# Performance work log

Hardware: AMD Instinct MI355X
Metric: run time of the kernel (lower is better)

Reference implementation:

```python
import jax, jax.numpy as jnp
import numpy as np

B, T, H = 2048, 200, 64
H1, H2 = 80, 40  # dnn_hidden_units


def setup_inputs() -> dict:
    key = jax.random.key(0)
    ks = jax.random.split(key, 9)
    query = jax.random.normal(ks[0], (B, H), dtype=jnp.float32)
    keys = jax.random.normal(ks[1], (B, T, H), dtype=jnp.float32)
    # lengths in [1, T] so every row has at least one valid key
    keys_length = jax.random.randint(ks[2], (B,), 1, T + 1, dtype=jnp.int32)
    s = 0.05  # weight scale (init_std in the repo is 1e-4; scaled up for numerics)
    W1 = jax.random.normal(ks[3], (4 * H, H1), dtype=jnp.float32) * s
    b1 = jnp.zeros((H1,), dtype=jnp.float32)
    W2 = jax.random.normal(ks[4], (H1, H2), dtype=jnp.float32) * s
    b2 = jnp.zeros((H2,), dtype=jnp.float32)
    Wfc = jax.random.normal(ks[5], (H2, 1), dtype=jnp.float32) * s
    bfc = jnp.zeros((1,), dtype=jnp.float32)
    return {"query": query, "keys": keys, "keys_length": keys_length,
            "W1": W1, "b1": b1, "W2": W2, "b2": b2, "Wfc": Wfc, "bfc": bfc}


def reference(query, keys, keys_length, W1, b1, W2, b2, Wfc, bfc):
    b, t, h = keys.shape
    qe = jnp.broadcast_to(query[:, None, :], keys.shape)          # [B,T,H]
    din = jnp.concatenate([qe, keys, qe - keys, qe * keys], -1)   # [B,T,4H]
    x = jax.nn.relu(jnp.einsum('btd,df->btf', din, W1) + b1)      # [B,T,H1]
    x = jax.nn.relu(jnp.einsum('btf,fg->btg', x, W2) + b2)        # [B,T,H2]
    scores = (jnp.einsum('btg,go->bto', x, Wfc) + bfc)[..., 0]    # [B,T]
    scores = scores / jnp.sqrt(jnp.float32(h))
    mask = jnp.arange(t)[None, :] < keys_length[:, None]          # [B,T]
    scores = jnp.where(mask, scores, -jnp.inf)
    attn = jax.nn.softmax(scores, axis=1)                         # [B,T]
    return jnp.einsum('bt,bth->bh', attn, keys)                   # [B,H]
```

## Files before the change

### kernel.cpp

```cpp
#include <hip/hip_runtime.h>
#include <math.h>

#define BB 2048
#define T  200
#define H  64
#define H1 80
#define H2 40

#define MT   13
#define TPAD 208
#define SA_STRIDE 72
#define SB1_STRIDE 72
#define SW_STRIDE 104
#define SB2_STRIDE 104

typedef __attribute__((ext_vector_type(8))) short short8;
typedef __attribute__((ext_vector_type(4))) float floatx4;

#define WS_WKT 0
#define WS_WPT (WS_WKT + H1 * H)
#define WS_WQ  (WS_WPT + H1 * H)
#define WS_W2T (WS_WQ + H * H1)

__device__ __forceinline__ unsigned short f2b(float x) {
    union { float f; unsigned u; } v; v.f = x;
    unsigned r = v.u + 0x7FFF + ((v.u >> 16) & 1);
    return (unsigned short)(r >> 16);
}
__device__ __forceinline__ float b2f(unsigned short u) {
    union { unsigned u; float f; } v; v.u = ((unsigned)u) << 16;
    return v.f;
}

__global__ void prep_kernel(const float* __restrict__ W1,
                            const float* __restrict__ W2,
                            float* __restrict__ ws) {
    int i = blockIdx.x * 256 + threadIdx.x;
    if (i < H1 * H) {
        int f = i / H, h = i % H;
        ws[WS_WKT + i] = W1[(64 + h) * H1 + f] - W1[(128 + h) * H1 + f];
        ws[WS_WPT + i] = W1[(192 + h) * H1 + f];
        ws[WS_WQ + h * H1 + f] = W1[h * H1 + f] + W1[(128 + h) * H1 + f];
    }
    if (i < 48 * SB2_STRIDE) {
        int n = i / SB2_STRIDE, k = i % SB2_STRIDE;
        float v = (n < H2 && k < H1) ? W2[k * H2 + n] : 0.f;
        ((unsigned short*)(ws + WS_W2T))[i] = f2b(v);
    }
}

__global__ __launch_bounds__(512, 4)
void din_attn_kernel(const float* __restrict__ query,
                     const float* __restrict__ keys,
                     const int*   __restrict__ keys_length,
                     const float* __restrict__ b1,
                     const float* __restrict__ b2,
                     const float* __restrict__ Wfc,
                     const float* __restrict__ bfc,
                     const float* __restrict__ ws,
                     float* __restrict__ out)
{
    __shared__ unsigned short sA[TPAD * SA_STRIDE];
    __shared__ unsigned short sHw[8][16 * SW_STRIDE];
    __shared__ unsigned short sB1[H1 * SB1_STRIDE];
    __shared__ float sQh[H1];
    __shared__ float sS[TPAD];
    __shared__ float sOut[8][H];
    __shared__ float sRed[16];

    const int b   = blockIdx.x;
    const int tid = threadIdx.x;
    const int wv  = tid >> 6, ln = tid & 63;
    const int lrow = ln & 15;
    const int lk8  = (ln >> 4) * 8;

    const float* kb = keys + (size_t)b * T * H;
    const float* qg = query + (size_t)b * H;

    const unsigned short* w2t = (const unsigned short*)(ws + WS_W2T);
    short8 b2frag[3][3];
    #pragma unroll
    for (int nt = 0; nt < 3; ++nt)
        #pragma unroll
        for (int ks = 0; ks < 3; ++ks)
            b2frag[nt][ks] = *reinterpret_cast<const short8*>(
                &w2t[(nt * 16 + lrow) * SB2_STRIDE + ks * 32 + lk8]);
    float wfcv[3], b2v[3];
    #pragma unroll
    for (int nt = 0; nt < 3; ++nt) {
        int g = nt * 16 + lrow;
        wfcv[nt] = (g < H2) ? Wfc[g] : 0.f;
        b2v[nt]  = (g < H2) ? b2[g]  : 0.f;
    }
    float bfc0 = bfc[0];
    int len = keys_length[b];

    for (int idx = tid; idx < T * H / 4; idx += 512) {
        float4 v = reinterpret_cast<const float4*>(kb)[idx];
        int t = idx >> 4, h = (idx & 15) << 2;
        uint2 p;
        p.x = (unsigned)f2b(v.x) | ((unsigned)f2b(v.y) << 16);
        p.y = (unsigned)f2b(v.z) | ((unsigned)f2b(v.w) << 16);
        *reinterpret_cast<uint2*>(&sA[t * SA_STRIDE + h]) = p;
    }
    for (int idx = tid; idx < 8 * SA_STRIDE / 2; idx += 512)
        reinterpret_cast<unsigned*>(&sA[200 * SA_STRIDE])[idx] = 0;
    for (int idx = tid; idx < H1 * H / 2; idx += 512) {
        int f = idx >> 5, hp = (idx & 31) << 1;
        float q0 = qg[hp], q1 = qg[hp + 1];
        float v0 = ws[WS_WKT + f * H + hp]     + q0 * ws[WS_WPT + f * H + hp];
        float v1 = ws[WS_WKT + f * H + hp + 1] + q1 * ws[WS_WPT + f * H + hp + 1];
        unsigned p = (unsigned)f2b(v0) | ((unsigned)f2b(v1) << 16);
        *reinterpret_cast<unsigned*>(&sB1[f * SB1_STRIDE + hp]) = p;
    }
    if (tid < H1) {
        float acc = b1[tid];
        #pragma unroll 8
        for (int h = 0; h < H; ++h) acc += qg[h] * ws[WS_WQ + h * H1 + tid];
        sQh[tid] = acc;
    }
    {
        uint2 z; z.x = 0; z.y = 0;
        *reinterpret_cast<uint2*>(&sHw[wv][lrow * SW_STRIDE + 80 + (ln >> 4) * 4]) = z;
    }
    __syncthreads();

    unsigned short* hw = &sHw[wv][0];
    #pragma unroll
    for (int mi = 0; mi < 2; ++mi) {
        int mt = wv + mi * 8;
        if (mt >= MT) break;
        short8 af[2];
        #pragma unroll
        for (int ks = 0; ks < 2; ++ks)
            af[ks] = *reinterpret_cast<const short8*>(
                &sA[(mt * 16 + lrow) * SA_STRIDE + ks * 32 + lk8]);
        #pragma unroll
        for (int nt = 0; nt < 5; ++nt) {
            short8 bf0 = *reinterpret_cast<const short8*>(
                &sB1[(nt * 16 + lrow) * SB1_STRIDE + lk8]);
            short8 bf1 = *reinterpret_cast<const short8*>(
                &sB1[(nt * 16 + lrow) * SB1_STRIDE + 32 + lk8]);
            floatx4 acc = {0.f, 0.f, 0.f, 0.f};
            acc = __builtin_amdgcn_mfma_f32_16x16x32_bf16(af[0], bf0, acc, 0, 0, 0);
            acc = __builtin_amdgcn_mfma_f32_16x16x32_bf16(af[1], bf1, acc, 0, 0, 0);
            float qh = sQh[nt * 16 + lrow];
            int rb = (ln >> 4) * 4;
            #pragma unroll
            for (int r = 0; r < 4; ++r)
                hw[(rb + r) * SW_STRIDE + nt * 16 + lrow] = f2b(fmaxf(acc[r] + qh, 0.f));
        }
        short8 a2[3];
        #pragma unroll
        for (int ks = 0; ks < 3; ++ks)
            a2[ks] = *reinterpret_cast<const short8*>(
                &hw[lrow * SW_STRIDE + ks * 32 + lk8]);
        floatx4 vsum = {0.f, 0.f, 0.f, 0.f};
        #pragma unroll
        for (int nt = 0; nt < 3; ++nt) {
            floatx4 acc = {0.f, 0.f, 0.f, 0.f};
            #pragma unroll
            for (int ks = 0; ks < 3; ++ks)
                acc = __builtin_amdgcn_mfma_f32_16x16x32_bf16(a2[ks], b2frag[nt][ks], acc, 0, 0, 0);
            #pragma unroll
            for (int r = 0; r < 4; ++r)
                vsum[r] += fmaxf(acc[r] + b2v[nt], 0.f) * wfcv[nt];
        }
        #pragma unroll
        for (int r = 0; r < 4; ++r) {
            vsum[r] += __shfl_xor(vsum[r], 1);
            vsum[r] += __shfl_xor(vsum[r], 2);
            vsum[r] += __shfl_xor(vsum[r], 4);
            vsum[r] += __shfl_xor(vsum[r], 8);
        }
        if (lrow == 0) {
            int tb = mt * 16 + (ln >> 4) * 4;
            #pragma unroll
            for (int r = 0; r < 4; ++r)
                sS[tb + r] = (vsum[r] + bfc0) * 0.125f;
        }
    }
    __syncthreads();

    float s = -INFINITY;
    if (tid < TPAD) s = (tid < len) ? sS[tid] : -INFINITY;
    float m = s;
    #pragma unroll
    for (int off = 32; off > 0; off >>= 1) m = fmaxf(m, __shfl_xor(m, off));
    if (ln == 0) sRed[wv] = m;
    __syncthreads();
    float mx = sRed[0];
    #pragma unroll
    for (int i = 1; i < 8; ++i) mx = fmaxf(mx, sRed[i]);
    float e = (tid < TPAD) ? __expf(s - mx) : 0.f;
    float sum = e;
    #pragma unroll
    for (int off = 32; off > 0; off >>= 1) sum += __shfl_xor(sum, off);
    if (ln == 0) sRed[8 + wv] = sum;
    __syncthreads();
    float denom = sRed[8];
    #pragma unroll
    for (int i = 1; i < 8; ++i) denom += sRed[8 + i];
    float inv = 1.f / denom;
    if (tid < TPAD) sS[tid] = e * inv;
    __syncthreads();

    float acc = 0.f;
    for (int t = wv * 26; t < wv * 26 + 26; ++t)
        acc += sS[t] * b2f(sA[t * SA_STRIDE + ln]);
    sOut[wv][ln] = acc;
    __syncthreads();
    if (tid < H) {
        float o = 0.f;
        #pragma unroll
        for (int g = 0; g < 8; ++g) o += sOut[g][tid];
        out[(size_t)b * H + tid] = o;
    }
}

extern "C" void kernel_launch(void* const* d_in, const int* in_sizes, int n_in,
                              void* d_out, int out_size, void* d_ws, size_t ws_size,
                              hipStream_t stream) {
    const float* query       = (const float*)d_in[0];
    const float* keys        = (const float*)d_in[1];
    const int*   keys_length = (const int*)  d_in[2];
    const float* W1          = (const float*)d_in[3];
    const float* b1          = (const float*)d_in[4];
    const float* W2          = (const float*)d_in[5];
    const float* b2          = (const float*)d_in[6];
    const float* Wfc         = (const float*)d_in[7];
    const float* bfc         = (const float*)d_in[8];
    float* out = (float*)d_out;
    float* ws  = (float*)d_ws;

    prep_kernel<<<20, 256, 0, stream>>>(W1, W2, ws);
    din_attn_kernel<<<BB, 512, 0, stream>>>(query, keys, keys_length,
                                            b1, b2, Wfc, bfc, ws, out);
}
```

Measured before the change: 60.36 us.

## Shrink LDS with XOR swizzle and buffer reuse to raise occupancy

```diff
diff --git a/kernel.cpp b/kernel.cpp
--- a/kernel.cpp
+++ b/kernel.cpp
@@ -9,10 +9,8 @@
 
 #define MT   13
 #define TPAD 208
-#define SA_STRIDE 72
-#define SB1_STRIDE 72
-#define SW_STRIDE 104
 #define SB2_STRIDE 104
+#define SCR_STRIDE 104
 
 typedef __attribute__((ext_vector_type(8))) short short8;
 typedef __attribute__((ext_vector_type(4))) float floatx4;
@@ -49,7 +47,7 @@
     }
 }
 
-__global__ __launch_bounds__(512, 4)
+__global__ __launch_bounds__(512, 6)
 void din_attn_kernel(const float* __restrict__ query,
                      const float* __restrict__ keys,
                      const int*   __restrict__ keys_length,
@@ -60,12 +58,10 @@
                      const float* __restrict__ ws,
                      float* __restrict__ out)
 {
-    __shared__ unsigned short sA[TPAD * SA_STRIDE];
-    __shared__ unsigned short sHw[8][16 * SW_STRIDE];
-    __shared__ unsigned short sB1[H1 * SB1_STRIDE];
+    __shared__ unsigned short sA[TPAD * 64];
+    __shared__ unsigned short sB1[H1 * 64];
     __shared__ float sQh[H1];
     __shared__ float sS[TPAD];
-    __shared__ float sOut[8][H];
     __shared__ float sRed[16];
 
     const int b   = blockIdx.x;
@@ -73,18 +69,12 @@
     const int wv  = tid >> 6, ln = tid & 63;
     const int lrow = ln & 15;
     const int lk8  = (ln >> 4) * 8;
+    const int sw   = (lrow & 7) << 3;
 
     const float* kb = keys + (size_t)b * T * H;
     const float* qg = query + (size_t)b * H;
-
     const unsigned short* w2t = (const unsigned short*)(ws + WS_W2T);
-    short8 b2frag[3][3];
-    #pragma unroll
-    for (int nt = 0; nt < 3; ++nt)
-        #pragma unroll
-        for (int ks = 0; ks < 3; ++ks)
-            b2frag[nt][ks] = *reinterpret_cast<const short8*>(
-                &w2t[(nt * 16 + lrow) * SB2_STRIDE + ks * 32 + lk8]);
+
     float wfcv[3], b2v[3];
     #pragma unroll
     for (int nt = 0; nt < 3; ++nt) {
@@ -95,23 +85,44 @@
     float bfc0 = bfc[0];
     int len = keys_length[b];
 
-    for (int idx = tid; idx < T * H / 4; idx += 512) {
-        float4 v = reinterpret_cast<const float4*>(kb)[idx];
+    const float4* kb4 = reinterpret_cast<const float4*>(kb);
+    float4 kv[6];
+    #pragma unroll
+    for (int k = 0; k < 6; ++k) kv[k] = kb4[tid + (k << 9)];
+    const bool tail = tid < (T * H / 4 - 3072);
+    float4 kvt;
+    if (tail) kvt = kb4[tid + 3072];
+
+    #pragma unroll
+    for (int k = 0; k < 6; ++k) {
+        int idx = tid + (k << 9);
         int t = idx >> 4, h = (idx & 15) << 2;
         uint2 p;
-        p.x = (unsigned)f2b(v.x) | ((unsigned)f2b(v.y) << 16);
-        p.y = (unsigned)f2b(v.z) | ((unsigned)f2b(v.w) << 16);
-        *reinterpret_cast<uint2*>(&sA[t * SA_STRIDE + h]) = p;
-    }
-    for (int idx = tid; idx < 8 * SA_STRIDE / 2; idx += 512)
-        reinterpret_cast<unsigned*>(&sA[200 * SA_STRIDE])[idx] = 0;
-    for (int idx = tid; idx < H1 * H / 2; idx += 512) {
+        p.x = (unsigned)f2b(kv[k].x) | ((unsigned)f2b(kv[k].y) << 16);
+        p.y = (unsigned)f2b(kv[k].z) | ((unsigned)f2b(kv[k].w) << 16);
+        *reinterpret_cast<uint2*>(&sA[t * 64 + (h ^ ((t & 7) << 3))]) = p;
+    }
+    if (tail) {
+        int idx = tid + 3072;
+        int t = idx >> 4, h = (idx & 15) << 2;
+        uint2 p;
+        p.x = (unsigned)f2b(kvt.x) | ((unsigned)f2b(kvt.y) << 16);
+        p.y = (unsigned)f2b(kvt.z) | ((unsigned)f2b(kvt.w) << 16);
+        *reinterpret_cast<uint2*>(&sA[t * 64 + (h ^ ((t & 7) << 3))]) = p;
+    }
+    if (tid < 64) {
+        uint4 z; z.x = z.y = z.z = z.w = 0;
+        reinterpret_cast<uint4*>(&sA[200 * 64])[tid] = z;
+    }
+    #pragma unroll
+    for (int k = 0; k < 5; ++k) {
+        int idx = tid + (k << 9);
         int f = idx >> 5, hp = (idx & 31) << 1;
         float q0 = qg[hp], q1 = qg[hp + 1];
         float v0 = ws[WS_WKT + f * H + hp]     + q0 * ws[WS_WPT + f * H + hp];
         float v1 = ws[WS_WKT + f * H + hp + 1] + q1 * ws[WS_WPT + f * H + hp + 1];
         unsigned p = (unsigned)f2b(v0) | ((unsigned)f2b(v1) << 16);
-        *reinterpret_cast<unsigned*>(&sB1[f * SB1_STRIDE + hp]) = p;
+        *reinterpret_cast<unsigned*>(&sB1[f * 64 + (hp ^ ((f & 7) << 3))]) = p;
     }
     if (tid < H1) {
         float acc = b1[tid];
@@ -119,49 +130,64 @@
         for (int h = 0; h < H; ++h) acc += qg[h] * ws[WS_WQ + h * H1 + tid];
         sQh[tid] = acc;
     }
+    __syncthreads();
+
+    short8 af[2][2];
+    bool has[2];
+    #pragma unroll
+    for (int mi = 0; mi < 2; ++mi) {
+        int mt = wv + mi * 8;
+        has[mi] = (mt < MT);
+        if (has[mi]) {
+            #pragma unroll
+            for (int ks = 0; ks < 2; ++ks) {
+                int row = mt * 16 + lrow;
+                af[mi][ks] = *reinterpret_cast<const short8*>(
+                    &sA[row * 64 + ((ks * 32 + lk8) ^ sw)]);
+            }
+        }
+    }
+    __syncthreads();
+
+    unsigned short* scr = &sA[wv * 16 * SCR_STRIDE];
     {
         uint2 z; z.x = 0; z.y = 0;
-        *reinterpret_cast<uint2*>(&sHw[wv][lrow * SW_STRIDE + 80 + (ln >> 4) * 4]) = z;
-    }
-    __syncthreads();
-
-    unsigned short* hw = &sHw[wv][0];
+        *reinterpret_cast<uint2*>(&scr[(ln >> 2) * SCR_STRIDE + 80 + (ln & 3) * 4]) = z;
+    }
+
     #pragma unroll
     for (int mi = 0; mi < 2; ++mi) {
+        if (!has[mi]) break;
         int mt = wv + mi * 8;
-        if (mt >= MT) break;
-        short8 af[2];
-        #pragma unroll
-        for (int ks = 0; ks < 2; ++ks)
-            af[ks] = *reinterpret_cast<const short8*>(
-                &sA[(mt * 16 + lrow) * SA_STRIDE + ks * 32 + lk8]);
         #pragma unroll
         for (int nt = 0; nt < 5; ++nt) {
-            short8 bf0 = *reinterpret_cast<const short8*>(
-                &sB1[(nt * 16 + lrow) * SB1_STRIDE + lk8]);
-            short8 bf1 = *reinterpret_cast<const short8*>(
-                &sB1[(nt * 16 + lrow) * SB1_STRIDE + 32 + lk8]);
+            int row = nt * 16 + lrow;
+            short8 bf0 = *reinterpret_cast<const short8*>(&sB1[row * 64 + (lk8 ^ sw)]);
+            short8 bf1 = *reinterpret_cast<const short8*>(&sB1[row * 64 + ((32 + lk8) ^ sw)]);
             floatx4 acc = {0.f, 0.f, 0.f, 0.f};
-            acc = __builtin_amdgcn_mfma_f32_16x16x32_bf16(af[0], bf0, acc, 0, 0, 0);
-            acc = __builtin_amdgcn_mfma_f32_16x16x32_bf16(af[1], bf1, acc, 0, 0, 0);
+            acc = __builtin_amdgcn_mfma_f32_16x16x32_bf16(af[mi][0], bf0, acc, 0, 0, 0);
+            acc = __builtin_amdgcn_mfma_f32_16x16x32_bf16(af[mi][1], bf1, acc, 0, 0, 0);
             float qh = sQh[nt * 16 + lrow];
             int rb = (ln >> 4) * 4;
             #pragma unroll
             for (int r = 0; r < 4; ++r)
-                hw[(rb + r) * SW_STRIDE + nt * 16 + lrow] = f2b(fmaxf(acc[r] + qh, 0.f));
+                scr[(rb + r) * SCR_STRIDE + nt * 16 + lrow] = f2b(fmaxf(acc[r] + qh, 0.f));
         }
         short8 a2[3];
         #pragma unroll
         for (int ks = 0; ks < 3; ++ks)
             a2[ks] = *reinterpret_cast<const short8*>(
-                &hw[lrow * SW_STRIDE + ks * 32 + lk8]);
+                &scr[lrow * SCR_STRIDE + ks * 32 + lk8]);
         floatx4 vsum = {0.f, 0.f, 0.f, 0.f};
         #pragma unroll
         for (int nt = 0; nt < 3; ++nt) {
             floatx4 acc = {0.f, 0.f, 0.f, 0.f};
             #pragma unroll
-            for (int ks = 0; ks < 3; ++ks)
-                acc = __builtin_amdgcn_mfma_f32_16x16x32_bf16(a2[ks], b2frag[nt][ks], acc, 0, 0, 0);
+            for (int ks = 0; ks < 3; ++ks) {
+                short8 b2frag = *reinterpret_cast<const short8*>(
+                    &w2t[(nt * 16 + lrow) * SB2_STRIDE + ks * 32 + lk8]);
+                acc = __builtin_amdgcn_mfma_f32_16x16x32_bf16(a2[ks], b2frag, acc, 0, 0, 0);
+            }
             #pragma unroll
             for (int r = 0; r < 4; ++r)
                 vsum[r] += fmaxf(acc[r] + b2v[nt], 0.f) * wfcv[nt];
@@ -205,15 +231,18 @@
     if (tid < TPAD) sS[tid] = e * inv;
     __syncthreads();
 
+    float* sOut = reinterpret_cast<float*>(sB1);
     float acc = 0.f;
-    for (int t = wv * 26; t < wv * 26 + 26; ++t)
-        acc += sS[t] * b2f(sA[t * SA_STRIDE + ln]);
-    sOut[wv][ln] = acc;
+    int t0 = wv * 26;
+    int tend = t0 + 26 < T ? t0 + 26 : T;
+    for (int t = t0; t < tend; ++t)
+        acc += sS[t] * kb[t * H + ln];
+    sOut[wv * 64 + ln] = acc;
     __syncthreads();
     if (tid < H) {
         float o = 0.f;
         #pragma unroll
-        for (int g = 0; g < 8; ++g) o += sOut[g][tid];
+        for (int g = 0; g < 8; ++g) o += sOut[g * 64 + tid];
         out[(size_t)b * H + tid] = o;
     }
 }
```

After: 72.71 us. +20.5%, slower.

## Split into flattened-token score kernel and separate softmax/weighted-sum kernel

Applied to the files above, without the earlier changes.

```diff
diff --git a/kernel.cpp b/kernel.cpp
--- a/kernel.cpp
+++ b/kernel.cpp
@@ -6,21 +6,18 @@
 #define H  64
 #define H1 80
 #define H2 40
-
-#define MT   13
-#define TPAD 208
-#define SA_STRIDE 72
-#define SB1_STRIDE 72
-#define SW_STRIDE 104
-#define SB2_STRIDE 104
+#define BT (BB * T)
+#define TILE 128
+#define NBLK (BT / TILE)
 
 typedef __attribute__((ext_vector_type(8))) short short8;
 typedef __attribute__((ext_vector_type(4))) float floatx4;
 
-#define WS_WKT 0
-#define WS_WPT (WS_WKT + H1 * H)
-#define WS_WQ  (WS_WPT + H1 * H)
-#define WS_W2T (WS_WQ + H * H1)
+#define WS_W2T_US 0
+#define WS_W1P_US (48 * 104)
+#define WS_US_END (WS_W1P_US + 80 * 128)
+#define WS_QH_F   (WS_US_END / 2)
+#define WS_SC_F   (WS_QH_F + BB * H1)
 
 __device__ __forceinline__ unsigned short f2b(float x) {
     union { float f; unsigned u; } v; v.f = x;
@@ -32,189 +29,234 @@
     return v.f;
 }
 
-__global__ void prep_kernel(const float* __restrict__ W1,
-                            const float* __restrict__ W2,
-                            float* __restrict__ ws) {
-    int i = blockIdx.x * 256 + threadIdx.x;
-    if (i < H1 * H) {
-        int f = i / H, h = i % H;
-        ws[WS_WKT + i] = W1[(64 + h) * H1 + f] - W1[(128 + h) * H1 + f];
-        ws[WS_WPT + i] = W1[(192 + h) * H1 + f];
-        ws[WS_WQ + h * H1 + f] = W1[h * H1 + f] + W1[(128 + h) * H1 + f];
-    }
-    if (i < 48 * SB2_STRIDE) {
-        int n = i / SB2_STRIDE, k = i % SB2_STRIDE;
+__global__ __launch_bounds__(256)
+void prep_kernel(const float* __restrict__ W1, const float* __restrict__ W2,
+                 const float* __restrict__ b1, const float* __restrict__ query,
+                 float* __restrict__ ws) {
+    int gid = blockIdx.x * 256 + threadIdx.x;
+    unsigned short* wsu = (unsigned short*)ws;
+    if (gid < 48 * 104) {
+        int n = gid / 104, k = gid % 104;
         float v = (n < H2 && k < H1) ? W2[k * H2 + n] : 0.f;
-        ((unsigned short*)(ws + WS_W2T))[i] = f2b(v);
-    }
-}
-
-__global__ __launch_bounds__(512, 4)
-void din_attn_kernel(const float* __restrict__ query,
-                     const float* __restrict__ keys,
-                     const int*   __restrict__ keys_length,
-                     const float* __restrict__ b1,
-                     const float* __restrict__ b2,
-                     const float* __restrict__ Wfc,
-                     const float* __restrict__ bfc,
+        wsu[WS_W2T_US + gid] = f2b(v);
+    }
+    if (gid < H1 * 128) {
+        int f = gid >> 7, k = gid & 127;
+        float v = (k < 64) ? W1[(64 + k) * H1 + f] - W1[(128 + k) * H1 + f]
+                           : W1[(192 + (k - 64)) * H1 + f];
+        wsu[WS_W1P_US + gid] = f2b(v);
+    }
+    int b = gid / H1, f = gid - b * H1;
+    const float* q = query + (size_t)b * H;
+    float acc = b1[f];
+    #pragma unroll 8
+    for (int h = 0; h < H; ++h)
+        acc += q[h] * (W1[h * H1 + f] + W1[(128 + h) * H1 + f]);
+    ws[WS_QH_F + gid] = acc;
+}
+
+__global__ __launch_bounds__(512, 6)
+void score_kernel(const float* __restrict__ query,
+                  const float* __restrict__ keys,
+                  const float* __restrict__ b2,
+                  const float* __restrict__ Wfc,
+                  const float* __restrict__ bfc,
+                  float* __restrict__ ws)
+{
+    __shared__ unsigned short sAS[13312];
+    __shared__ unsigned short sB1[80 * 128];
+    __shared__ unsigned short sQb[128];
+    __shared__ float sQh2[160];
+
+    const int tid = threadIdx.x;
+    const int wv = tid >> 6, ln = tid & 63;
+    const int lrow = ln & 15;
+    const int lk8 = (ln >> 4) * 8;
+    const int bt0 = blockIdx.x * TILE;
+    const int b0 = bt0 / T;
+    const int bsplit = (b0 + 1) * T;
+    const int bnext = (b0 + 1 < BB) ? b0 + 1 : b0;
+
+    const float4* kb4 = reinterpret_cast<const float4*>(keys) + (size_t)bt0 * (H / 4);
+    #pragma unroll
+    for (int kk = 0; kk < 4; ++kk) {
+        int idx = tid + (kk << 9);
+        float4 v = kb4[idx];
+        int row = idx >> 4, seg = idx & 15;
+        int chunk = seg >> 1, half = seg & 1;
+        uint2 p;
+        p.x = (unsigned)f2b(v.x) | ((unsigned)f2b(v.y) << 16);
+        p.y = (unsigned)f2b(v.z) | ((unsigned)f2b(v.w) << 16);
+        *reinterpret_cast<uint2*>(
+            &sAS[row * 64 + ((chunk ^ (row & 7)) << 3) + (half << 2)]) = p;
+    }
+    const uint4* w1p4 = reinterpret_cast<const uint4*>(
+        (const unsigned short*)ws + WS_W1P_US);
+    #pragma unroll
+    for (int kk = 0; kk < 3; ++kk) {
+        int i = tid + (kk << 9);
+        if (i < 1280) {
+            uint4 v = w1p4[i];
+            int row = i >> 4, c = i & 15;
+            *reinterpret_cast<uint4*>(&sB1[row * 128 + ((c ^ (row & 7)) << 3)]) = v;
+        }
+    }
+    if (tid < 128) {
+        int which = tid >> 6, h = tid & 63;
+        int bq = which ? bnext : b0;
+        sQb[tid] = f2b(query[(size_t)bq * H + h]);
+    }
+    if (tid < 160) {
+        int which = (tid >= 80), f = tid - which * 80;
+        int bq = which ? bnext : b0;
+        sQh2[tid] = ws[WS_QH_F + bq * H1 + f];
+    }
+    __syncthreads();
+
+    const int mrow = wv * 16 + lrow;
+    const int selL = (bt0 + mrow >= bsplit) ? 1 : 0;
+    short8 af[2], af23[2];
+    #pragma unroll
+    for (int ks = 0; ks < 2; ++ks) {
+        int c = ks * 4 + (ln >> 4);
+        af[ks] = *reinterpret_cast<const short8*>(
+            &sAS[mrow * 64 + ((c ^ (mrow & 7)) << 3)]);
+        short8 aq = *reinterpret_cast<const short8*>(&sQb[selL * 64 + ks * 32 + lk8]);
+        #pragma unroll
+        for (int j = 0; j < 8; ++j)
+            af23[ks][j] = (short)f2b(
+                b2f((unsigned short)af[ks][j]) * b2f((unsigned short)aq[j]));
+    }
+    __syncthreads();
+
+    unsigned short* scr = &sAS[wv * 1664];
+    {
+        uint2 z; z.x = 0; z.y = 0;
+        *reinterpret_cast<uint2*>(&scr[(ln >> 2) * 104 + 80 + (ln & 3) * 4]) = z;
+    }
+
+    const int rb = (ln >> 4) * 4;
+    const int c0 = (ln >> 4);
+    #pragma unroll
+    for (int nt = 0; nt < 5; ++nt) {
+        int brow = nt * 16 + lrow;
+        floatx4 acc = {0.f, 0.f, 0.f, 0.f};
+        short8 bf;
+        bf = *reinterpret_cast<const short8*>(
+            &sB1[brow * 128 + (((0 + c0) ^ (brow & 7)) << 3)]);
+        acc = __builtin_amdgcn_mfma_f32_16x16x32_bf16(af[0], bf, acc, 0, 0, 0);
+        bf = *reinterpret_cast<const short8*>(
+            &sB1[brow * 128 + (((4 + c0) ^ (brow & 7)) << 3)]);
+        acc = __builtin_amdgcn_mfma_f32_16x16x32_bf16(af[1], bf, acc, 0, 0, 0);
+        bf = *reinterpret_cast<const short8*>(
+            &sB1[brow * 128 + (((8 + c0) ^ (brow & 7)) << 3)]);
+        acc = __builtin_amdgcn_mfma_f32_16x16x32_bf16(af23[0], bf, acc, 0, 0, 0);
+        bf = *reinterpret_cast<const short8*>(
+            &sB1[brow * 128 + (((12 + c0) ^ (brow & 7)) << 3)]);
+        acc = __builtin_amdgcn_mfma_f32_16x16x32_bf16(af23[1], bf, acc, 0, 0, 0);
+        #pragma unroll
+        for (int r = 0; r < 4; ++r) {
+            int sel = (bt0 + wv * 16 + rb + r >= bsplit) ? 1 : 0;
+            float qh = sQh2[sel * 80 + nt * 16 + lrow];
+            scr[(rb + r) * 104 + nt * 16 + lrow] = f2b(fmaxf(acc[r] + qh, 0.f));
+        }
+    }
+
+    const unsigned short* w2t = (const unsigned short*)ws + WS_W2T_US;
+    float bfc0 = bfc[0];
+    short8 a2[3];
+    #pragma unroll
+    for (int ks = 0; ks < 3; ++ks)
+        a2[ks] = *reinterpret_cast<const short8*>(&scr[lrow * 104 + ks * 32 + lk8]);
+    floatx4 vsum = {0.f, 0.f, 0.f, 0.f};
+    #pragma unroll
+    for (int nt = 0; nt < 3; ++nt) {
+        int g = nt * 16 + lrow;
+        float wf = (g < H2) ? Wfc[g] : 0.f;
+        float bb = (g < H2) ? b2[g] : 0.f;
+        floatx4 acc = {0.f, 0.f, 0.f, 0.f};
+        #pragma unroll
+        for (int ks = 0; ks < 3; ++ks) {
+            short8 b2f8 = *reinterpret_cast<const short8*>(
+                &w2t[g * 104 + ks * 32 + lk8]);
+            acc = __builtin_amdgcn_mfma_f32_16x16x32_bf16(a2[ks], b2f8, acc, 0, 0, 0);
+        }
+        #pragma unroll
+        for (int r = 0; r < 4; ++r)
+            vsum[r] += fmaxf(acc[r] + bb, 0.f) * wf;
+    }
+    #pragma unroll
+    for (int r = 0; r < 4; ++r) {
+        vsum[r] += __shfl_xor(vsum[r], 1);
+        vsum[r] += __shfl_xor(vsum[r], 2);
+        vsum[r] += __shfl_xor(vsum[r], 4);
+        vsum[r] += __shfl_xor(vsum[r], 8);
+    }
+    if (lrow == 0) {
+        #pragma unroll
+        for (int r = 0; r < 4; ++r) {
+            int btR = bt0 + wv * 16 + rb + r;
+            int bR = btR / T;
+            int tR = btR - bR * T;
+            ws[WS_SC_F + bR * 256 + tR] = (vsum[r] + bfc0) * 0.125f;
+        }
+    }
+}
+
+__global__ __launch_bounds__(256)
+void attn_out_kernel(const float* __restrict__ keys,
+                     const int* __restrict__ keys_length,
                      const float* __restrict__ ws,
                      float* __restrict__ out)
 {
-    __shared__ unsigned short sA[TPAD * SA_STRIDE];
-    __shared__ unsigned short sHw[8][16 * SW_STRIDE];
-    __shared__ unsigned short sB1[H1 * SB1_STRIDE];
-    __shared__ float sQh[H1];
-    __shared__ float sS[TPAD];
-    __shared__ float sOut[8][H];
-    __shared__ float sRed[16];
-
-    const int b   = blockIdx.x;
+    __shared__ float sS[256];
+    __shared__ float sRed[8];
+    __shared__ float sOutp[4][64];
+    const int b = blockIdx.x;
     const int tid = threadIdx.x;
-    const int wv  = tid >> 6, ln = tid & 63;
-    const int lrow = ln & 15;
-    const int lk8  = (ln >> 4) * 8;
-
-    const float* kb = keys + (size_t)b * T * H;
-    const float* qg = query + (size_t)b * H;
-
-    const unsigned short* w2t = (const unsigned short*)(ws + WS_W2T);
-    short8 b2frag[3][3];
-    #pragma unroll
-    for (int nt = 0; nt < 3; ++nt)
-        #pragma unroll
-        for (int ks = 0; ks < 3; ++ks)
-            b2frag[nt][ks] = *reinterpret_cast<const short8*>(
-                &w2t[(nt * 16 + lrow) * SB2_STRIDE + ks * 32 + lk8]);
-    float wfcv[3], b2v[3];
-    #pragma unroll
-    for (int nt = 0; nt < 3; ++nt) {
-        int g = nt * 16 + lrow;
-        wfcv[nt] = (g < H2) ? Wfc[g] : 0.f;
-        b2v[nt]  = (g < H2) ? b2[g]  : 0.f;
-    }
-    float bfc0 = bfc[0];
-    int len = keys_length[b];
-
-    for (int idx = tid; idx < T * H / 4; idx += 512) {
-        float4 v = reinterpret_cast<const float4*>(kb)[idx];
-        int t = idx >> 4, h = (idx & 15) << 2;
-        uint2 p;
-        p.x = (unsigned)f2b(v.x) | ((unsigned)f2b(v.y) << 16);
-        p.y = (unsigned)f2b(v.z) | ((unsigned)f2b(v.w) << 16);
-        *reinterpret_cast<uint2*>(&sA[t * SA_STRIDE + h]) = p;
-    }
-    for (int idx = tid; idx < 8 * SA_STRIDE / 2; idx += 512)
-        reinterpret_cast<unsigned*>(&sA[200 * SA_STRIDE])[idx] = 0;
-    for (int idx = tid; idx < H1 * H / 2; idx += 512) {
-        int f = idx >> 5, hp = (idx & 31) << 1;
-        float q0 = qg[hp], q1 = qg[hp + 1];
-        float v0 = ws[WS_WKT + f * H + hp]     + q0 * ws[WS_WPT + f * H + hp];
-        float v1 = ws[WS_WKT + f * H + hp + 1] + q1 * ws[WS_WPT + f * H + hp + 1];
-        unsigned p = (unsigned)f2b(v0) | ((unsigned)f2b(v1) << 16);
-        *reinterpret_cast<unsigned*>(&sB1[f * SB1_STRIDE + hp]) = p;
-    }
-    if (tid < H1) {
-        float acc = b1[tid];
-        #pragma unroll 8
-        for (int h = 0; h < H; ++h) acc += qg[h] * ws[WS_WQ + h * H1 + tid];
-        sQh[tid] = acc;
-    }
-    {
-        uint2 z; z.x = 0; z.y = 0;
-        *reinterpret_cast<uint2*>(&sHw[wv][lrow * SW_STRIDE + 80 + (ln >> 4) * 4]) = z;
-    }
-    __syncthreads();
-
-    unsigned short* hw = &sHw[wv][0];
-    #pragma unroll
-    for (int mi = 0; mi < 2; ++mi) {
-        int mt = wv + mi * 8;
-        if (mt >= MT) break;
-        short8 af[2];
-        #pragma unroll
-        for (int ks = 0; ks < 2; ++ks)
-            af[ks] = *reinterpret_cast<const short8*>(
-                &sA[(mt * 16 + lrow) * SA_STRIDE + ks * 32 + lk8]);
-        #pragma unroll
-        for (int nt = 0; nt < 5; ++nt) {
-            short8 bf0 = *reinterpret_cast<const short8*>(
-                &sB1[(nt * 16 + lrow) * SB1_STRIDE + lk8]);
-            short8 bf1 = *reinterpret_cast<const short8*>(
-                &sB1[(nt * 16 + lrow) * SB1_STRIDE + 32 + lk8]);
-            floatx4 acc = {0.f, 0.f, 0.f, 0.f};
-            acc = __builtin_amdgcn_mfma_f32_16x16x32_bf16(af[0], bf0, acc, 0, 0, 0);
-            acc = __builtin_amdgcn_mfma_f32_16x16x32_bf16(af[1], bf1, acc, 0, 0, 0);
-            float qh = sQh[nt * 16 + lrow];
-            int rb = (ln >> 4) * 4;
-            #pragma unroll
-            for (int r = 0; r < 4; ++r)
-                hw[(rb + r) * SW_STRIDE + nt * 16 + lrow] = f2b(fmaxf(acc[r] + qh, 0.f));
-        }
-        short8 a2[3];
-        #pragma unroll
-        for (int ks = 0; ks < 3; ++ks)
-            a2[ks] = *reinterpret_cast<const short8*>(
-                &hw[lrow * SW_STRIDE + ks * 32 + lk8]);
-        floatx4 vsum = {0.f, 0.f, 0.f, 0.f};
-        #pragma unroll
-        for (int nt = 0; nt < 3; ++nt) {
-            floatx4 acc = {0.f, 0.f, 0.f, 0.f};
-            #pragma unroll
-            for (int ks = 0; ks < 3; ++ks)
-                acc = __builtin_amdgcn_mfma_f32_16x16x32_bf16(a2[ks], b2frag[nt][ks], acc, 0, 0, 0);
-            #pragma unroll
-            for (int r = 0; r < 4; ++r)
-                vsum[r] += fmaxf(acc[r] + b2v[nt], 0.f) * wfcv[nt];
-        }
-        #pragma unroll
-        for (int r = 0; r < 4; ++r) {
-            vsum[r] += __shfl_xor(vsum[r], 1);
-            vsum[r] += __shfl_xor(vsum[r], 2);
-            vsum[r] += __shfl_xor(vsum[r], 4);
-            vsum[r] += __shfl_xor(vsum[r], 8);
-        }
-        if (lrow == 0) {
-            int tb = mt * 16 + (ln >> 4) * 4;
-            #pragma unroll
-            for (int r = 0; r < 4; ++r)
-                sS[tb + r] = (vsum[r] + bfc0) * 0.125f;
-        }
-    }
-    __syncthreads();
+    const int wv = tid >> 6, ln = tid & 63;
+    const int len = keys_length[b];
 
     float s = -INFINITY;
-    if (tid < TPAD) s = (tid < len) ? sS[tid] : -INFINITY;
+    if (tid < len) s = ws[WS_SC_F + b * 256 + tid];
     float m = s;
     #pragma unroll
     for (int off = 32; off > 0; off >>= 1) m = fmaxf(m, __shfl_xor(m, off));
     if (ln == 0) sRed[wv] = m;
     __syncthreads();
-    float mx = sRed[0];
-    #pragma unroll
-    for (int i = 1; i < 8; ++i) mx = fmaxf(mx, sRed[i]);
-    float e = (tid < TPAD) ? __expf(s - mx) : 0.f;
+    float mx = fmaxf(fmaxf(sRed[0], sRed[1]), fmaxf(sRed[2], sRed[3]));
+    float e = (tid < len) ? __expf(s - mx) : 0.f;
+    sS[tid] = e;
     float sum = e;
     #pragma unroll
     for (int off = 32; off > 0; off >>= 1) sum += __shfl_xor(sum, off);
-    if (ln == 0) sRed[8 + wv] = sum;
-    __syncthreads();
-    float denom = sRed[8];
-    #pragma unroll
-    for (int i = 1; i < 8; ++i) denom += sRed[8 + i];
+    if (ln == 0) sRed[4 + wv] = sum;
+    __syncthreads();
+    float denom = (sRed[4] + sRed[5]) + (sRed[6] + sRed[7]);
     float inv = 1.f / denom;
-    if (tid < TPAD) sS[tid] = e * inv;
-    __syncthreads();
-
-    float acc = 0.f;
-    for (int t = wv * 26; t < wv * 26 + 26; ++t)
-        acc += sS[t] * b2f(sA[t * SA_STRIDE + ln]);
-    sOut[wv][ln] = acc;
+
+    const float* kb = keys + (size_t)b * T * H;
+    int h4 = (ln & 15) * 4;
+    int tg = wv * 4 + (ln >> 4);
+    float4 a; a.x = a.y = a.z = a.w = 0.f;
+    #pragma unroll
+    for (int i = 0; i < 13; ++i) {
+        int t = tg * 13 + i;
+        if (t < T) {
+            float w = sS[t];
+            float4 kv = *reinterpret_cast<const float4*>(&kb[t * H + h4]);
+            a.x += w * kv.x; a.y += w * kv.y; a.z += w * kv.z; a.w += w * kv.w;
+        }
+    }
+    a.x += __shfl_xor(a.x, 16); a.y += __shfl_xor(a.y, 16);
+    a.z += __shfl_xor(a.z, 16); a.w += __shfl_xor(a.w, 16);
+    a.x += __shfl_xor(a.x, 32); a.y += __shfl_xor(a.y, 32);
+    a.z += __shfl_xor(a.z, 32); a.w += __shfl_xor(a.w, 32);
+    if (ln < 16) *reinterpret_cast<float4*>(&sOutp[wv][h4]) = a;
     __syncthreads();
     if (tid < H) {
-        float o = 0.f;
-        #pragma unroll
-        for (int g = 0; g < 8; ++g) o += sOut[g][tid];
-        out[(size_t)b * H + tid] = o;
+        float o = (sOutp[0][tid] + sOutp[1][tid]) + (sOutp[2][tid] + sOutp[3][tid]);
+        out[(size_t)b * H + tid] = o * inv;
     }
 }
 
@@ -233,7 +275,7 @@
     float* out = (float*)d_out;
     float* ws  = (float*)d_ws;
 
-    prep_kernel<<<20, 256, 0, stream>>>(W1, W2, ws);
-    din_attn_kernel<<<BB, 512, 0, stream>>>(query, keys, keys_length,
-                                            b1, b2, Wfc, bfc, ws, out);
-}
+    prep_kernel<<<640, 256, 0, stream>>>(W1, W2, b1, query, ws);
+    score_kernel<<<NBLK, 512, 0, stream>>>(query, keys, b2, Wfc, bfc, ws);
+    attn_out_kernel<<<BB, 256, 0, stream>>>(keys, keys_length, ws, out);
+}
```

Result: slower. 62.03 us (+2.8%).
